# Optimization experiments

Hardware: AMD Instinct MI355X
Metric: run time of the kernel (lower is better)

## Reference

```python
import jax, jax.numpy as jnp
import numpy as np

B, S, D, H = 2, 2048, 512, 8
DK = D // H
MASK_VALUE = -1e9


def setup_inputs() -> dict:
    key = jax.random.key(0)
    ks = jax.random.split(key, 12)
    scale = 1.0 / np.sqrt(D)
    inp = {
        "query": jax.random.normal(ks[0], (B, S, D), jnp.float32),
        "key": jax.random.normal(ks[1], (B, S, D), jnp.float32),
        "value": jax.random.normal(ks[2], (B, S, D), jnp.float32),
        # causal mask, broadcastable over batch and heads
        "mask": jnp.tril(jnp.ones((S, S), jnp.int32))[None, None, :, :],
        "Wq": jax.random.normal(ks[3], (D, D), jnp.float32) * scale,
        "bq": jax.random.normal(ks[4], (D,), jnp.float32) * scale,
        "Wk": jax.random.normal(ks[5], (D, D), jnp.float32) * scale,
        "bk": jax.random.normal(ks[6], (D,), jnp.float32) * scale,
        "Wv": jax.random.normal(ks[7], (D, D), jnp.float32) * scale,
        "bv": jax.random.normal(ks[8], (D,), jnp.float32) * scale,
        "Wo": jax.random.normal(ks[9], (D, D), jnp.float32) * scale,
        "bo": jax.random.normal(ks[10], (D,), jnp.float32) * scale,
    }
    return inp


def reference(query, key, value, mask, Wq, bq, Wk, bk, Wv, bv, Wo, bo):
    # linear projections (torch Linear: x @ W.T + b)
    q = query @ Wq.T + bq
    k = key @ Wk.T + bk
    v = value @ Wv.T + bv
    # split heads: [B,S,D] -> [B,H,S,DK]
    q = q.reshape(B, S, H, DK).transpose(0, 2, 1, 3)
    k = k.reshape(B, S, H, DK).transpose(0, 2, 1, 3)
    v = v.reshape(B, S, H, DK).transpose(0, 2, 1, 3)
    # scaled dot-product attention with explicit [B,H,S,S] score matrix
    scores = jnp.einsum("bhqd,bhkd->bhqk", q, k) / jnp.sqrt(jnp.float32(DK))
    scores = jnp.where(mask == 0, jnp.float32(MASK_VALUE), scores)
    attn = jax.nn.softmax(scores, axis=-1)
    x = jnp.einsum("bhqk,bhkd->bhqd", attn, v)
    # merge heads: [B,H,S,DK] -> [B,S,D]
    x = x.transpose(0, 2, 1, 3).reshape(B, S, D)
    return x @ Wo.T + bo
```

## Files before the change

kernel.cpp:

```cpp
#include <hip/hip_runtime.h>
#include <hip/hip_bf16.h>

#define B_   2
#define S_   2048
#define D_   512
#define H_   8
#define DK_  64
#define M_   (B_*S_)

typedef float  floatx4 __attribute__((ext_vector_type(4)));
typedef __bf16 bf16x8  __attribute__((ext_vector_type(8)));

#define MFMA16x16x32(a,b,c) __builtin_amdgcn_mfma_f32_16x16x32_bf16((a),(b),(c),0,0,0)

static __device__ __forceinline__ void load_lds16(const void* g, void* l) {
  __builtin_amdgcn_global_load_lds(
      (const __attribute__((address_space(1))) void*)g,
      (__attribute__((address_space(3))) void*)l,
      16, 0, 0);
}

__global__ __launch_bounds__(256) void cvt_inputs(
    const float* __restrict__ w0, const float* __restrict__ w1,
    const float* __restrict__ w2, const float* __restrict__ w3,
    const float* __restrict__ x0, const float* __restrict__ x1,
    const float* __restrict__ x2,
    __bf16* __restrict__ out)
{
  const int idx = (blockIdx.x * 256 + threadIdx.x) * 4;
  const float* src;
  int off;
  if (idx < 1048576) {
    src = (idx < 524288) ? ((idx < 262144) ? w0 : w1)
                         : ((idx < 786432) ? w2 : w3);
    off = idx & 0x3FFFF;
  } else {
    const int i2 = idx - 1048576;
    const int xs = i2 >> 21;
    src = (xs == 0) ? x0 : (xs == 1) ? x1 : x2;
    off = i2 & 0x1FFFFF;
  }
  float4 v = *(const float4*)(src + off);
  __bf16* o = out + idx;
  o[0]=(__bf16)v.x; o[1]=(__bf16)v.y; o[2]=(__bf16)v.z; o[3]=(__bf16)v.w;
}


__global__ __launch_bounds__(256) void proj_qkv(
    const __bf16* __restrict__ Xb, const __bf16* __restrict__ Wball,
    const float* __restrict__ bq, const float* __restrict__ bk, const float* __restrict__ bv,
    __bf16* __restrict__ Qb, __bf16* __restrict__ Kb, __bf16* __restrict__ Vtb)
{
  __shared__ __align__(16) __bf16 smem[12288];

  const int z = blockIdx.z;
  const __bf16* X    = Xb + (size_t)z * (M_*D_);
  const __bf16* W    = Wball + (size_t)z * (D_*D_);
  const float*  bias = (z==0) ? bq : (z==1) ? bk : bv;

  const int m0 = blockIdx.x * 64;
  const int n0 = blockIdx.y * 128;
  const int tid  = threadIdx.x;
  const int w    = tid >> 6;
  const int lane = tid & 63;
  const int lcol = lane & 15;
  const int quad = lane >> 4;
  const int wm = w & 1, wn = w >> 1;

  floatx4 zero = {0.f,0.f,0.f,0.f};
  floatx4 acc[2][4];
#pragma unroll
  for (int i = 0; i < 2; ++i)
#pragma unroll
    for (int nt = 0; nt < 4; ++nt) acc[i][nt] = zero;

  auto stage = [&](int bsel, int k0) {
    {
      const int u = w*64 + lane;
      load_lds16(X + (size_t)(m0 + (u >> 2))*D_ + k0 + (u & 3)*8,
                 (char*)(smem + bsel*2048) + w*1024);
    }
#pragma unroll
    for (int j = 0; j < 2; ++j) {
      const int u = (j*4 + w)*64 + lane;
      load_lds16(W + (size_t)(n0 + (u >> 2))*D_ + k0 + (u & 3)*8,
                 (char*)(smem + 4096 + bsel*4096) + (j*4 + w)*1024);
    }
  };

  stage(0, 0);
  for (int it = 0; it < 16; ++it) {
    __syncthreads();
    if (it + 1 < 16) stage((it+1)&1, (it+1)*32);
    const __bf16* ab = smem + (it&1)*2048;
    const __bf16* bb = smem + 4096 + (it&1)*4096;
    bf16x8 af[2], bf[4];
#pragma unroll
    for (int i = 0; i < 2; ++i)
      af[i] = *(const bf16x8*)(ab + (wm*32 + i*16 + lcol)*32 + quad*8);
#pragma unroll
    for (int nt = 0; nt < 4; ++nt)
      bf[nt] = *(const bf16x8*)(bb + (wn*64 + nt*16 + lcol)*32 + quad*8);
#pragma unroll
    for (int i = 0; i < 2; ++i)
#pragma unroll
      for (int nt = 0; nt < 4; ++nt)
        acc[i][nt] = MFMA16x16x32(af[i], bf[nt], acc[i][nt]);
  }

  __syncthreads();
#pragma unroll
  for (int nt = 0; nt < 4; ++nt) {
    const int n = n0 + wn*64 + nt*16 + lcol;
    const float bias_n = bias[n];
    const int h_l = (n >> 6) & 1;
    const int dk  = n & 63;
#pragma unroll
    for (int i = 0; i < 2; ++i)
#pragma unroll
      for (int r = 0; r < 4; ++r) {
        const int m = m0 + wm*32 + i*16 + quad*4 + r;
        const float val = acc[i][nt][r] + bias_n;
        const int klo = m & 63;
        int off;
        if (z == 0) {
          off = klo*64 + dk;
        } else if (z == 1) {
          off = (((klo>>4)*2 + (dk>>5))*64 + ((dk>>3)&3)*16 + (klo&15))*8 + (dk&7);
        } else {
          off = (((dk>>4)*2 + (klo>>5))*64 + ((klo>>3)&3)*16 + (dk&15))*8 + (klo&7);
        }
        smem[h_l*4096 + off] = (__bf16)val;
      }
  }
  __syncthreads();

  __bf16* dst = (z==0) ? Qb : (z==1) ? Kb : Vtb;
  const int bb2 = m0 >> 11;
  const int hh0 = n0 >> 6;
  const int cc0 = (m0 & 2047) >> 6;
#pragma unroll
  for (int it2 = 0; it2 < 4; ++it2) {
    const int u = it2*256 + tid;
    const int p = u >> 9, o = u & 511;
    const size_t base = ((size_t)(bb2*H_ + hh0 + p))*(S_*DK_) + (size_t)cc0*4096;
    *(bf16x8*)(dst + base + o*8) = *(const bf16x8*)(smem + p*4096 + o*8);
  }
}

__global__ __launch_bounds__(256, 2) void attn_fwd(
    const __bf16* __restrict__ Qb, const __bf16* __restrict__ Kb,
    const __bf16* __restrict__ Vtb, __bf16* __restrict__ attnb)
{
  __shared__ __align__(16) __bf16 pbuf[4][16*72];

  const int tid  = threadIdx.x;
  const int w    = tid >> 6;
  const int lane = tid & 63;
  const int lcol = lane & 15;
  const int quad = lane >> 4;
  const int hh = blockIdx.y;
  const int bb = blockIdx.z;

  const int t   = 127 - (blockIdx.x*4 + w);
  const int qr0 = t * 16;

  const __bf16* Qp = Qb  + (size_t)(bb*H_ + hh) * S_ * DK_;
  const __bf16* Kp = Kb  + (size_t)(bb*H_ + hh) * S_ * DK_;
  const __bf16* Vp = Vtb + (size_t)(bb*H_ + hh) * DK_ * S_;

  const bf16x8 aq0 = *(const bf16x8*)(Qp + (size_t)(qr0 + lcol)*DK_ + quad*8);
  const bf16x8 aq1 = *(const bf16x8*)(Qp + (size_t)(qr0 + lcol)*DK_ + 32 + quad*8);

  floatx4 zero = {0.f,0.f,0.f,0.f};
  floatx4 acc[4] = {zero, zero, zero, zero};
  float lsum[4] = {0.f, 0.f, 0.f, 0.f};

  bf16x8 kA[8], vA[8], kB[8], vB[8];

  auto ld = [&](bf16x8 (&kf)[8], bf16x8 (&vf)[8], int c) {
    const __bf16* kp = Kp + (size_t)c*4096 + lane*8;
    const __bf16* vp = Vp + (size_t)c*4096 + lane*8;
#pragma unroll
    for (int i = 0; i < 8; ++i) kf[i] = *(const bf16x8*)(kp + i*512);
#pragma unroll
    for (int i = 0; i < 8; ++i) vf[i] = *(const bf16x8*)(vp + i*512);
  };

  auto compute = [&](const bf16x8 (&kc)[8], const bf16x8 (&vc)[8],
                     int k0, bool edge) {
    floatx4 s[4];
#pragma unroll
    for (int nt = 0; nt < 4; ++nt)
      s[nt] = MFMA16x16x32(aq1, kc[nt*2+1], MFMA16x16x32(aq0, kc[nt*2+0], zero));
#pragma unroll
    for (int nt = 0; nt < 4; ++nt) {
#pragma unroll
      for (int r = 0; r < 4; ++r) {
        float p = exp2f(s[nt][r] * 0.18033688011112042f);
        if (edge) {
          const int qrow = qr0 + quad*4 + r;
          if (k0 + nt*16 + lcol > qrow) p = 0.f;
        }
        lsum[r] += p;
        pbuf[w][(quad*4 + r)*72 + nt*16 + lcol] = (__bf16)p;
      }
    }
    asm volatile("s_waitcnt lgkmcnt(0)" ::: "memory");
    const bf16x8 pa0 = *(const bf16x8*)(&pbuf[w][lcol*72 + quad*8]);
    const bf16x8 pa1 = *(const bf16x8*)(&pbuf[w][lcol*72 + 32 + quad*8]);
#pragma unroll
    for (int nt = 0; nt < 4; ++nt) {
      acc[nt] = MFMA16x16x32(pa0, vc[nt*2+0], acc[nt]);
      acc[nt] = MFMA16x16x32(pa1, vc[nt*2+1], acc[nt]);
    }
  };

  const int nch = (t >> 2) + 1;
  ld(kA, vA, 0);
  for (int c = 0; c + 1 < nch; ++c) {
    if (c & 1) { ld(kA, vA, c+1); compute(kB, vB, c*64, false); }
    else       { ld(kB, vB, c+1); compute(kA, vA, c*64, false); }
  }
  if ((nch - 1) & 1) compute(kB, vB, (nch-1)*64, true);
  else               compute(kA, vA, (nch-1)*64, true);

  float rinv[4];
#pragma unroll
  for (int r = 0; r < 4; ++r) {
    float tv = lsum[r];
    tv += __shfl_xor(tv, 1, 16);
    tv += __shfl_xor(tv, 2, 16);
    tv += __shfl_xor(tv, 4, 16);
    tv += __shfl_xor(tv, 8, 16);
    rinv[r] = 1.0f / tv;
  }

#pragma unroll
  for (int nt = 0; nt < 4; ++nt)
#pragma unroll
    for (int r = 0; r < 4; ++r) {
      const int q = qr0 + quad*4 + r;
      attnb[((size_t)(bb*S_ + q)) * D_ + hh*DK_ + nt*16 + lcol] =
          (__bf16)(acc[nt][r] * rinv[r]);
    }
}

__global__ __launch_bounds__(256) void proj_out(
    const __bf16* __restrict__ attnb, const __bf16* __restrict__ Wob,
    const float* __restrict__ bo, float* __restrict__ out)
{
  __shared__ __align__(16) __bf16 smem[12288];

  const int m0 = blockIdx.x * 64;
  const int n0 = blockIdx.y * 128;
  const int tid  = threadIdx.x;
  const int w    = tid >> 6;
  const int lane = tid & 63;
  const int lcol = lane & 15;
  const int quad = lane >> 4;
  const int wm = w & 1, wn = w >> 1;

  floatx4 zero = {0.f,0.f,0.f,0.f};
  floatx4 acc[2][4];
#pragma unroll
  for (int i = 0; i < 2; ++i)
#pragma unroll
    for (int nt = 0; nt < 4; ++nt) acc[i][nt] = zero;

  auto stage = [&](int bsel, int k0) {
    {
      const int u = w*64 + lane;
      load_lds16(attnb + (size_t)(m0 + (u >> 2))*D_ + k0 + (u & 3)*8,
                 (char*)(smem + bsel*2048) + w*1024);
    }
#pragma unroll
    for (int j = 0; j < 2; ++j) {
      const int u = (j*4 + w)*64 + lane;
      load_lds16(Wob + (size_t)(n0 + (u >> 2))*D_ + k0 + (u & 3)*8,
                 (char*)(smem + 4096 + bsel*4096) + (j*4 + w)*1024);
    }
  };

  stage(0, 0);
  for (int it = 0; it < 16; ++it) {
    __syncthreads();
    if (it + 1 < 16) stage((it+1)&1, (it+1)*32);
    const __bf16* ab = smem + (it&1)*2048;
    const __bf16* bb = smem + 4096 + (it&1)*4096;
    bf16x8 af[2], bf[4];
#pragma unroll
    for (int i = 0; i < 2; ++i)
      af[i] = *(const bf16x8*)(ab + (wm*32 + i*16 + lcol)*32 + quad*8);
#pragma unroll
    for (int nt = 0; nt < 4; ++nt)
      bf[nt] = *(const bf16x8*)(bb + (wn*64 + nt*16 + lcol)*32 + quad*8);
#pragma unroll
    for (int i = 0; i < 2; ++i)
#pragma unroll
      for (int nt = 0; nt < 4; ++nt)
        acc[i][nt] = MFMA16x16x32(af[i], bf[nt], acc[i][nt]);
  }

#pragma unroll
  for (int nt = 0; nt < 4; ++nt) {
    const int n = n0 + wn*64 + nt*16 + lcol;
    const float bias_n = bo[n];
#pragma unroll
    for (int i = 0; i < 2; ++i)
#pragma unroll
      for (int r = 0; r < 4; ++r) {
        const int m = m0 + wm*32 + i*16 + quad*4 + r;
        out[(size_t)m * D_ + n] = acc[i][nt][r] + bias_n;
      }
  }
}

extern "C" void kernel_launch(void* const* d_in, const int* in_sizes, int n_in,
                              void* d_out, int out_size, void* d_ws, size_t ws_size,
                              hipStream_t stream) {
  const float* q_in = (const float*)d_in[0];
  const float* k_in = (const float*)d_in[1];
  const float* v_in = (const float*)d_in[2];
  const float* Wq = (const float*)d_in[4];
  const float* bq = (const float*)d_in[5];
  const float* Wk = (const float*)d_in[6];
  const float* bk = (const float*)d_in[7];
  const float* Wv = (const float*)d_in[8];
  const float* bv = (const float*)d_in[9];
  const float* Wo = (const float*)d_in[10];
  const float* bo = (const float*)d_in[11];
  float* out = (float*)d_out;

  __bf16* ws    = (__bf16*)d_ws;
  __bf16* Qb    = ws;
  __bf16* Kb    = ws + 1*2097152;
  __bf16* Vtb   = ws + 2*2097152;
  __bf16* attnb = ws + 3*2097152;
  __bf16* Wb    = ws + 4*2097152;
  __bf16* Xb    = Wb + 4*262144;

  cvt_inputs<<<dim3(7168), dim3(256), 0, stream>>>(
      Wq, Wk, Wv, Wo, q_in, k_in, v_in, Wb);

  proj_qkv<<<dim3(M_/64, D_/128, 3), dim3(256), 0, stream>>>(
      Xb, Wb, bq, bk, bv, Qb, Kb, Vtb);

  attn_fwd<<<dim3(32, H_, B_), dim3(256), 0, stream>>>(Qb, Kb, Vtb, attnb);

  proj_out<<<dim3(M_/64, D_/128), dim3(256), 0, stream>>>(
      attnb, Wb + 3*262144, bo, out);
}
```

Measured before the change: 189.7 us.

## Share K/V chunks across warps via LDS double-buffering in attention

Each block now handles 64 consecutive query rows, with the four warps sharing K and V chunks staged into double-buffered LDS via global_load_lds, instead of each warp loading its own copy into registers. This cuts redundant global/L2 traffic for K/V and lowers register pressure. Query tile ordering is reversed for one batch to balance causal work across blocks. In exchange, it adds a block-wide barrier per chunk and partially masked work for some warps on the diagonal chunk.

```diff
diff --git a/kernel.cpp b/kernel.cpp
--- a/kernel.cpp
+++ b/kernel.cpp
@@ -148,10 +148,12 @@
   }
 }
 
-__global__ __launch_bounds__(256, 2) void attn_fwd(
+__global__ __launch_bounds__(256) void attn_fwd(
     const __bf16* __restrict__ Qb, const __bf16* __restrict__ Kb,
     const __bf16* __restrict__ Vtb, __bf16* __restrict__ attnb)
 {
+  __shared__ __align__(16) __bf16 kbuf[2][4096];
+  __shared__ __align__(16) __bf16 vbuf[2][4096];
   __shared__ __align__(16) __bf16 pbuf[4][16*72];
 
   const int tid  = threadIdx.x;
@@ -162,8 +164,9 @@
   const int hh = blockIdx.y;
   const int bb = blockIdx.z;
 
-  const int t   = 127 - (blockIdx.x*4 + w);
-  const int qr0 = t * 16;
+  const int t   = (bb == 0) ? (31 - (int)blockIdx.x) : (int)blockIdx.x;
+  const int q0  = t * 64;
+  const int qr0 = q0 + w*16;
 
   const __bf16* Qp = Qb  + (size_t)(bb*H_ + hh) * S_ * DK_;
   const __bf16* Kp = Kb  + (size_t)(bb*H_ + hh) * S_ * DK_;
@@ -176,23 +179,36 @@
   floatx4 acc[4] = {zero, zero, zero, zero};
   float lsum[4] = {0.f, 0.f, 0.f, 0.f};
 
-  bf16x8 kA[8], vA[8], kB[8], vB[8];
-
-  auto ld = [&](bf16x8 (&kf)[8], bf16x8 (&vf)[8], int c) {
-    const __bf16* kp = Kp + (size_t)c*4096 + lane*8;
-    const __bf16* vp = Vp + (size_t)c*4096 + lane*8;
-#pragma unroll
-    for (int i = 0; i < 8; ++i) kf[i] = *(const bf16x8*)(kp + i*512);
-#pragma unroll
-    for (int i = 0; i < 8; ++i) vf[i] = *(const bf16x8*)(vp + i*512);
+  auto stage_chunk = [&](int bsel, int c) {
+    const char* ksrc = (const char*)(Kp + (size_t)c * 4096);
+    const char* vsrc = (const char*)(Vp + (size_t)c * 4096);
+#pragma unroll
+    for (int j = 0; j < 2; ++j) {
+      const int off = w*2048 + j*1024;
+      load_lds16(ksrc + off + lane*16, (char*)kbuf[bsel] + off);
+      load_lds16(vsrc + off + lane*16, (char*)vbuf[bsel] + off);
+    }
   };
 
-  auto compute = [&](const bf16x8 (&kc)[8], const bf16x8 (&vc)[8],
-                     int k0, bool edge) {
+  const int nch = t + 1;
+  stage_chunk(0, 0);
+  for (int c = 0; c < nch; ++c) {
+    __syncthreads();
+    if (c + 1 < nch) stage_chunk((c+1)&1, c+1);
+    const int bsel = c & 1;
+    const int k0 = c * 64;
+    const __bf16* kb = kbuf[bsel];
+    const __bf16* vb = vbuf[bsel];
+
     floatx4 s[4];
 #pragma unroll
-    for (int nt = 0; nt < 4; ++nt)
-      s[nt] = MFMA16x16x32(aq1, kc[nt*2+1], MFMA16x16x32(aq0, kc[nt*2+0], zero));
+    for (int nt = 0; nt < 4; ++nt) {
+      bf16x8 kf0 = *(const bf16x8*)(kb + (nt*2+0)*512 + lane*8);
+      bf16x8 kf1 = *(const bf16x8*)(kb + (nt*2+1)*512 + lane*8);
+      s[nt] = MFMA16x16x32(aq1, kf1, MFMA16x16x32(aq0, kf0, zero));
+    }
+
+    const bool edge = (k0 + 63 > qr0);
 #pragma unroll
     for (int nt = 0; nt < 4; ++nt) {
 #pragma unroll
@@ -207,23 +223,17 @@
       }
     }
     asm volatile("s_waitcnt lgkmcnt(0)" ::: "memory");
+
     const bf16x8 pa0 = *(const bf16x8*)(&pbuf[w][lcol*72 + quad*8]);
     const bf16x8 pa1 = *(const bf16x8*)(&pbuf[w][lcol*72 + 32 + quad*8]);
 #pragma unroll
     for (int nt = 0; nt < 4; ++nt) {
-      acc[nt] = MFMA16x16x32(pa0, vc[nt*2+0], acc[nt]);
-      acc[nt] = MFMA16x16x32(pa1, vc[nt*2+1], acc[nt]);
-    }
-  };
-
-  const int nch = (t >> 2) + 1;
-  ld(kA, vA, 0);
-  for (int c = 0; c + 1 < nch; ++c) {
-    if (c & 1) { ld(kA, vA, c+1); compute(kB, vB, c*64, false); }
-    else       { ld(kB, vB, c+1); compute(kA, vA, c*64, false); }
-  }
-  if ((nch - 1) & 1) compute(kB, vB, (nch-1)*64, true);
-  else               compute(kA, vA, (nch-1)*64, true);
+      bf16x8 vf0 = *(const bf16x8*)(vb + (nt*2+0)*512 + lane*8);
+      bf16x8 vf1 = *(const bf16x8*)(vb + (nt*2+1)*512 + lane*8);
+      acc[nt] = MFMA16x16x32(pa0, vf0, acc[nt]);
+      acc[nt] = MFMA16x16x32(pa1, vf1, acc[nt]);
+    }
+  }
 
   float rinv[4];
 #pragma unroll
```

Result: faster. 171.3 us (-9.7%).
